# Optimization experiments

Measured on AMD Instinct MI355X. Metric: run time of the kernel, lower is better.

## Reference

```python
import jax, jax.numpy as jnp
import numpy as np

GRID_SIZE = 8
SPLINE_ORDER = 3
LAYERS = [256, 512, 512, 256]  # [input_dim] + hidden_dims
BATCH = 8192
BN_EPS = 1e-5


def make_grid(in_features):
    # efficient-kan/torchkan grid: uniform on [-1, 1] extended by spline_order on each side
    h = 2.0 / GRID_SIZE
    g = jnp.arange(-SPLINE_ORDER, GRID_SIZE + SPLINE_ORDER + 1, dtype=jnp.float32) * h - 1.0
    return jnp.broadcast_to(g, (in_features, g.shape[0]))  # (In, G + 2k + 1)


def b_splines(x, grid):
    # x: (B, In), grid: (In, G + 2k + 1) -> bases: (B, In, G + k)
    xg = x[:, :, None]
    bases = ((xg >= grid[:, :-1]) & (xg < grid[:, 1:])).astype(x.dtype)
    for k in range(1, SPLINE_ORDER + 1):
        left = (xg - grid[:, : -(k + 1)]) / (grid[:, k:-1] - grid[:, : -(k + 1)])
        right = (grid[:, k + 1 :] - xg) / (grid[:, k + 1 :] - grid[:, 1:-k])
        bases = left * bases[:, :, :-1] + right * bases[:, :, 1:]
    return bases


def kan_linear(x, grid, base_w, spline_w):
    # base path: GELU (exact, matching torch.nn.GELU) then linear
    base_out = jax.nn.gelu(x, approximate=False) @ base_w.T
    spline_out = jnp.einsum('bik,oik->bo', b_splines(x, grid), spline_w)
    return base_out + spline_out


def setup_inputs() -> dict:
    key = jax.random.key(0)
    ks = jax.random.split(key, 16)
    inp = {'x': jax.random.normal(ks[0], (BATCH, LAYERS[0]), dtype=jnp.float32)}
    n_bases = GRID_SIZE + SPLINE_ORDER
    for i, (fin, fout) in enumerate(zip(LAYERS[:-1], LAYERS[1:])):
        scale = 1.0 / np.sqrt(fin)
        inp[f'grid{i}'] = make_grid(fin)
        inp[f'base_w{i}'] = jax.random.normal(ks[1 + 3 * i], (fout, fin), dtype=jnp.float32) * scale
        inp[f'spline_w{i}'] = jax.random.normal(ks[2 + 3 * i], (fout, fin, n_bases), dtype=jnp.float32) * (0.1 * scale)
    d_out = LAYERS[-1]
    inp['bn_gamma'] = jnp.ones((d_out,), dtype=jnp.float32)
    inp['bn_beta'] = jnp.zeros((d_out,), dtype=jnp.float32)
    inp['bn_mean'] = jax.random.normal(ks[10], (d_out,), dtype=jnp.float32) * 0.1
    inp['bn_var'] = jax.random.uniform(ks[11], (d_out,), dtype=jnp.float32, minval=0.5, maxval=1.5)
    return inp


def reference(x, grid0, base_w0, spline_w0, grid1, base_w1, spline_w1, grid2, base_w2, spline_w2, bn_gamma, bn_beta, bn_mean, bn_var):
    h = kan_linear(x, grid0, base_w0, spline_w0)
    h = kan_linear(h, grid1, base_w1, spline_w1)
    h = kan_linear(h, grid2, base_w2, spline_w2)
    # BatchNorm1d in eval mode (running stats); Dropout is identity at inference
    return bn_gamma * (h - bn_mean) * jax.lax.rsqrt(bn_var + BN_EPS) + bn_beta
```

## Files before the change

kernel.cpp:

```cpp
#include <hip/hip_runtime.h>
#include <hip/hip_bf16.h>
#include <cstdint>


typedef unsigned short ushort_t;
typedef __bf16 bf16x8 __attribute__((ext_vector_type(8)));
typedef float f32x4 __attribute__((ext_vector_type(4)));
typedef _Float16 f16x4 __attribute__((ext_vector_type(4)));

__device__ __forceinline__ ushort_t f2bf(float f) {
    __bf16 h = (__bf16)f;
    return __builtin_bit_cast(ushort_t, h);
}

__device__ __forceinline__ void gload_lds16(const void* g, void* lds) {
    __builtin_amdgcn_global_load_lds(
        (const __attribute__((address_space(1))) unsigned int*)(uintptr_t)g,
        (__attribute__((address_space(3))) unsigned int*)(unsigned int)(uintptr_t)lds,
        16, 0, 0);
}

__device__ __forceinline__ void expand12(float x, ushort_t* o) {
    float x3 = x * x * x;
    float y  = 0.7978845608028654f * (x + 0.044715f * x3);
    float e  = __expf(2.0f * y);
    float th = 1.0f - 2.0f / (e + 1.0f);
    o[0] = f2bf(0.5f * x * (1.0f + th));
    float xs = (x + 1.75f) * 4.0f;
#pragma unroll
    for (int j = 0; j < 11; ++j) {
        float t  = xs - (float)j;
        float a  = fabsf(t - 2.0f);
        float p1 = (3.0f * a - 6.0f) * a * a + 4.0f;
        float c  = 2.0f - a;
        float p2 = c * c * c;
        float v  = (a <= 1.0f) ? p1 : fmaxf(p2, 0.0f);
        o[1 + j] = f2bf(v * (1.0f / 6.0f));
    }
}

__global__ __launch_bounds__(256) void expand_kernel(
    const float* __restrict__ X0, ushort_t* __restrict__ A, int total2)
{
    int idx = blockIdx.x * 256 + threadIdx.x;
    if (idx >= total2) return;
    float2 h = *(const float2*)(X0 + 2 * (size_t)idx);
    union { ushort_t us[24]; uint4 v[3]; } pk;
    expand12(h.x, pk.us);
    expand12(h.y, pk.us + 12);
    uint4* dst = (uint4*)(A + (size_t)idx * 24);
    dst[0] = pk.v[0]; dst[1] = pk.v[1]; dst[2] = pk.v[2];
}

__global__ __launch_bounds__(256) void expand_sum_kernel(
    const _Float16* __restrict__ P, size_t pstride,
    ushort_t* __restrict__ A, int total4)
{
    int idx = blockIdx.x * 256 + threadIdx.x;
    if (idx >= total4) return;
    float h0 = 0.f, h1 = 0.f, h2 = 0.f, h3 = 0.f;
#pragma unroll
    for (int s = 0; s < 4; ++s) {
        f16x4 v = *(const f16x4*)(P + s * pstride + 4 * (size_t)idx);
        h0 += (float)v.x; h1 += (float)v.y; h2 += (float)v.z; h3 += (float)v.w;
    }
    union { ushort_t us[48]; uint4 v[6]; } pk;
    expand12(h0, pk.us);
    expand12(h1, pk.us + 12);
    expand12(h2, pk.us + 24);
    expand12(h3, pk.us + 36);
    uint4* dst = (uint4*)(A + (size_t)idx * 48);
#pragma unroll
    for (int i = 0; i < 6; ++i) dst[i] = pk.v[i];
}

__global__ __launch_bounds__(256) void pack_w_kernel(
    const float* __restrict__ bw, const float* __restrict__ sw,
    ushort_t* __restrict__ W, int total)
{
    int idx = blockIdx.x * 256 + threadIdx.x;
    if (idx >= total) return;
    union { ushort_t us[12]; uint2 v[3]; } pk;
    pk.us[0] = f2bf(bw[idx]);
    const float* s = sw + (size_t)idx * 11;
#pragma unroll
    for (int k = 0; k < 11; ++k) pk.us[1 + k] = f2bf(s[k]);
    uint2* dst = (uint2*)(W + (size_t)idx * 12);
    dst[0] = pk.v[0]; dst[1] = pk.v[1]; dst[2] = pk.v[2];
}

#define SLOTE 16384

__global__ __launch_bounds__(512, 2) void gemm_kernel(
    const ushort_t* __restrict__ A,
    const ushort_t* __restrict__ W,
    _Float16* __restrict__ C,
    int M, int N, int K, int scps)
{
    extern __shared__ __align__(16) ushort_t lds[];

    const int t   = threadIdx.x;
    const int l   = t & 63;
    const int w   = t >> 6;
    const int wm  = w >> 2;
    const int wn  = w & 3;
    const int l15 = l & 15;
    const int q   = l >> 4;
    const int blockM = blockIdx.x * 256;
    const int blockN = blockIdx.y * 256;
    const int kb0 = blockIdx.z * scps;
    const int nt  = scps;
    _Float16* Cz = C + (size_t)blockIdx.z * M * N;

    const ushort_t* Ab = A + (size_t)blockM * K;
    const ushort_t* Wb = W + (size_t)blockN * K;

    auto stage = [&](int kb, int slot) {
        ushort_t* da = lds + slot * SLOTE;
        ushort_t* db = da + 8192;
#pragma unroll
        for (int it = 0; it < 2; ++it) {
            int s = it * 512 + t;
            int row = s >> 2, g = (s & 3) ^ ((row >> 1) & 3);
            gload_lds16(Ab + ((size_t)row * K + (kb << 5) + g * 8), da + s * 8);
        }
#pragma unroll
        for (int it = 0; it < 2; ++it) {
            int s = it * 512 + t;
            int row = s >> 2, g = (s & 3) ^ ((row >> 1) & 3);
            gload_lds16(Wb + ((size_t)row * K + (kb << 5) + g * 8), db + s * 8);
        }
    };

    auto ldfrags = [&](int slot, bf16x8* afr, bf16x8* bfr) {
        const ushort_t* Ac = lds + slot * SLOTE;
        const ushort_t* Bc = Ac + 8192;
#pragma unroll
        for (int ni = 0; ni < 4; ++ni) {
            int n = wn * 64 + ni * 16 + l15;
            bfr[ni] = *(const bf16x8*)&Bc[(size_t)((n << 2) + (q ^ ((n >> 1) & 3))) * 8];
        }
#pragma unroll
        for (int mi = 0; mi < 8; ++mi) {
            int m = wm * 128 + mi * 16 + l15;
            afr[mi] = *(const bf16x8*)&Ac[(size_t)((m << 2) + (q ^ ((m >> 1) & 3))) * 8];
        }
    };

    f32x4 acc[8][4];
#pragma unroll
    for (int i = 0; i < 8; ++i)
#pragma unroll
        for (int j = 0; j < 4; ++j) acc[i][j] = (f32x4){0.f, 0.f, 0.f, 0.f};

    stage(kb0 + 0, 0); stage(kb0 + 1, 1); stage(kb0 + 2, 2);
    asm volatile("s_waitcnt vmcnt(4)" ::: "memory");
    __builtin_amdgcn_s_barrier();

    bf16x8 aA[8], bA[4], aB[8], bB[4];
    ldfrags(0, aA, bA);
    asm volatile("s_waitcnt lgkmcnt(0)" ::: "memory");

    auto body = [&](int tt, bf16x8* ac, bf16x8* bc, bf16x8* an, bf16x8* bn) {
        if (tt + 3 < nt) stage(kb0 + tt + 3, (tt + 3) & 3);
        if (tt + 1 < nt) ldfrags((tt + 1) & 3, an, bn);
        __builtin_amdgcn_sched_barrier(0);
        __builtin_amdgcn_s_setprio(1);
#pragma unroll
        for (int mi = 0; mi < 8; ++mi)
#pragma unroll
            for (int ni = 0; ni < 4; ++ni)
                acc[mi][ni] = __builtin_amdgcn_mfma_f32_16x16x32_bf16(
                    ac[mi], bc[ni], acc[mi][ni], 0, 0, 0);
        __builtin_amdgcn_s_setprio(0);
        asm volatile("s_waitcnt lgkmcnt(0)" ::: "memory");
        if (tt + 3 < nt)      asm volatile("s_waitcnt vmcnt(4)" ::: "memory");
        else if (tt + 2 < nt) asm volatile("s_waitcnt vmcnt(0)" ::: "memory");
        __builtin_amdgcn_s_barrier();
    };

    for (int tt = 0; tt < nt; tt += 2) {
        body(tt,     aA, bA, aB, bB);
        body(tt + 1, aB, bB, aA, bA);
    }

#pragma unroll
    for (int ni = 0; ni < 4; ++ni) {
        int n = blockN + wn * 64 + ni * 16 + l15;
#pragma unroll
        for (int mi = 0; mi < 8; ++mi) {
            int mb = blockM + wm * 128 + mi * 16 + q * 4;
#pragma unroll
            for (int r = 0; r < 4; ++r)
                Cz[(size_t)(mb + r) * N + n] = (_Float16)acc[mi][ni][r];
        }
    }
}

__global__ __launch_bounds__(256) void bn_reduce_kernel(
    const _Float16* __restrict__ Q, size_t qstride,
    const float* __restrict__ gamma, const float* __restrict__ beta,
    const float* __restrict__ mean,  const float* __restrict__ var,
    float4* __restrict__ out, int n4)
{
    int i = blockIdx.x * 256 + threadIdx.x;
    if (i >= n4) return;
    float sx = 0.f, sy = 0.f, sz = 0.f, sw = 0.f;
#pragma unroll
    for (int s = 0; s < 8; ++s) {
        f16x4 v = *(const f16x4*)(Q + s * qstride + 4 * (size_t)i);
        sx += (float)v.x; sy += (float)v.y; sz += (float)v.z; sw += (float)v.w;
    }
    int nb = (i * 4) & 255;
    float4 g  = *(const float4*)(gamma + nb);
    float4 be = *(const float4*)(beta + nb);
    float4 mn = *(const float4*)(mean + nb);
    float4 vr = *(const float4*)(var + nb);
    float4 o;
    o.x = g.x * rsqrtf(vr.x + 1e-5f) * (sx - mn.x) + be.x;
    o.y = g.y * rsqrtf(vr.y + 1e-5f) * (sy - mn.y) + be.y;
    o.z = g.z * rsqrtf(vr.z + 1e-5f) * (sz - mn.z) + be.z;
    o.w = g.w * rsqrtf(vr.w + 1e-5f) * (sw - mn.w) + be.w;
    out[i] = o;
}

extern "C" void kernel_launch(void* const* d_in, const int* in_sizes, int n_in,
                              void* d_out, int out_size, void* d_ws, size_t ws_size,
                              hipStream_t stream) {
    const float* x     = (const float*)d_in[0];
    const float* bw0   = (const float*)d_in[2];
    const float* sw0   = (const float*)d_in[3];
    const float* bw1   = (const float*)d_in[5];
    const float* sw1   = (const float*)d_in[6];
    const float* bw2   = (const float*)d_in[8];
    const float* sw2   = (const float*)d_in[9];
    const float* gamma = (const float*)d_in[10];
    const float* beta  = (const float*)d_in[11];
    const float* mean  = (const float*)d_in[12];
    const float* var   = (const float*)d_in[13];

    char* ws = (char*)d_ws;
    ushort_t*  Abuf = (ushort_t*)(ws);
    ushort_t*  W0   = (ushort_t*)(ws + 100663296);
    ushort_t*  W1   = (ushort_t*)(ws + 103809024);
    ushort_t*  W2   = (ushort_t*)(ws + 110100480);
    _Float16*  P    = (_Float16*)(ws + 113246208);
    float*     out  = (float*)d_out;

    const size_t PS01 = (size_t)8192 * 512;
    const size_t PS2  = (size_t)8192 * 256;
    const size_t GEMM_LDS = 4 * SLOTE * sizeof(ushort_t);

    pack_w_kernel<<<(512 * 256 + 255) / 256, 256, 0, stream>>>(bw0, sw0, W0, 512 * 256);
    pack_w_kernel<<<(512 * 512 + 255) / 256, 256, 0, stream>>>(bw1, sw1, W1, 512 * 512);
    pack_w_kernel<<<(256 * 512 + 255) / 256, 256, 0, stream>>>(bw2, sw2, W2, 256 * 512);

    expand_kernel<<<4096, 256, 0, stream>>>(x, Abuf, 8192 * 256 / 2);
    {
        dim3 g(32, 2, 4);
        gemm_kernel<<<g, 512, GEMM_LDS, stream>>>(Abuf, W0, P, 8192, 512, 3072, 24);
    }
    expand_sum_kernel<<<4096, 256, 0, stream>>>(P, PS01, Abuf, 8192 * 512 / 4);
    {
        dim3 g(32, 2, 4);
        gemm_kernel<<<g, 512, GEMM_LDS, stream>>>(Abuf, W1, P, 8192, 512, 6144, 48);
    }
    expand_sum_kernel<<<4096, 256, 0, stream>>>(P, PS01, Abuf, 8192 * 512 / 4);
    {
        dim3 g(32, 1, 8);
        gemm_kernel<<<g, 512, GEMM_LDS, stream>>>(Abuf, W2, P, 8192, 256, 6144, 24);
    }
    bn_reduce_kernel<<<2048, 256, 0, stream>>>(
        P, PS2, gamma, beta, mean, var, (float4*)out, 8192 * 256 / 4);
}
```

Before: 326.3 us.

## Store expanded activation in K-block tiled panels for contiguous GEMM staging

The expand kernels now write the bf16 basis-expanded activation as 256-row by 32-column tiles, contiguous per K-block, instead of row-major. Each GEMM stage then reads one contiguous 16KB chunk for A rather than 256 rows strided by K, which should improve DRAM and TLB locality for the global-to-LDS loads. The expand kernel is reworked so each thread emits exactly one 32-element chunk. That chunk straddles feature boundaries and needs 3 or 4 feature expansions, so some expansion work is recomputed and the expand kernel's input reads become less coalesced.

```diff
diff --git a/kernel.cpp b/kernel.cpp
--- a/kernel.cpp
+++ b/kernel.cpp
@@ -39,39 +39,58 @@
     }
 }
 
-__global__ __launch_bounds__(256) void expand_kernel(
-    const float* __restrict__ X0, ushort_t* __restrict__ A, int total2)
-{
-    int idx = blockIdx.x * 256 + threadIdx.x;
-    if (idx >= total2) return;
-    float2 h = *(const float2*)(X0 + 2 * (size_t)idx);
-    union { ushort_t us[24]; uint4 v[3]; } pk;
-    expand12(h.x, pk.us);
-    expand12(h.y, pk.us + 12);
-    uint4* dst = (uint4*)(A + (size_t)idx * 24);
-    dst[0] = pk.v[0]; dst[1] = pk.v[1]; dst[2] = pk.v[2];
-}
-
-__global__ __launch_bounds__(256) void expand_sum_kernel(
-    const _Float16* __restrict__ P, size_t pstride,
-    ushort_t* __restrict__ A, int total4)
-{
-    int idx = blockIdx.x * 256 + threadIdx.x;
-    if (idx >= total4) return;
+__device__ __forceinline__ void pack32(const ushort_t* s, uint4* o) {
+#pragma unroll
+    for (int c = 0; c < 4; ++c) {
+        o[c].x = (unsigned)s[c * 8 + 0] | ((unsigned)s[c * 8 + 1] << 16);
+        o[c].y = (unsigned)s[c * 8 + 2] | ((unsigned)s[c * 8 + 3] << 16);
+        o[c].z = (unsigned)s[c * 8 + 4] | ((unsigned)s[c * 8 + 5] << 16);
+        o[c].w = (unsigned)s[c * 8 + 6] | ((unsigned)s[c * 8 + 7] << 16);
+    }
+}
+
+template <int KB, bool FROMX>
+__global__ __launch_bounds__(256) void expand_tiled_kernel(
+    const float* __restrict__ X, const _Float16* __restrict__ P,
+    size_t pstride, ushort_t* __restrict__ A)
+{
+    constexpr int F = KB * 8 / 3;
+    const int idx = blockIdx.x * 256 + threadIdx.x;
+    const int row = idx & 255;
+    const int pkb = idx >> 8;
+    const int kb  = pkb % KB;
+    const int p   = pkb / KB;
+    const int b   = p * 256 + row;
+    const int i0  = (kb * 8) / 3;
+    const int cse = kb - 3 * (kb / 3);
+
     float h0 = 0.f, h1 = 0.f, h2 = 0.f, h3 = 0.f;
-#pragma unroll
-    for (int s = 0; s < 4; ++s) {
-        f16x4 v = *(const f16x4*)(P + s * pstride + 4 * (size_t)idx);
-        h0 += (float)v.x; h1 += (float)v.y; h2 += (float)v.z; h3 += (float)v.w;
-    }
-    union { ushort_t us[48]; uint4 v[6]; } pk;
-    expand12(h0, pk.us);
-    expand12(h1, pk.us + 12);
-    expand12(h2, pk.us + 24);
-    expand12(h3, pk.us + 36);
-    uint4* dst = (uint4*)(A + (size_t)idx * 48);
-#pragma unroll
-    for (int i = 0; i < 6; ++i) dst[i] = pk.v[i];
+    if (FROMX) {
+        const float* xr = X + (size_t)b * F + i0;
+        h0 = xr[0]; h1 = xr[1]; h2 = xr[2];
+        if (cse == 1) h3 = xr[3];
+    } else {
+#pragma unroll
+        for (int z = 0; z < 4; ++z) {
+            const _Float16* pr = P + z * pstride + (size_t)b * F + i0;
+            h0 += (float)pr[0]; h1 += (float)pr[1]; h2 += (float)pr[2];
+            if (cse == 1) h3 += (float)pr[3];
+        }
+    }
+
+    ushort_t us[48];
+    expand12(h0, us);
+    expand12(h1, us + 12);
+    expand12(h2, us + 24);
+    if (cse == 1) expand12(h3, us + 36);
+
+    uint4 o[4];
+    if (cse == 0)      pack32(us + 0, o);
+    else if (cse == 1) pack32(us + 8, o);
+    else               pack32(us + 4, o);
+
+    uint4* dst = (uint4*)(A + (size_t)idx * 32);
+    dst[0] = o[0]; dst[1] = o[1]; dst[2] = o[2]; dst[3] = o[3];
 }
 
 __global__ __launch_bounds__(256) void pack_w_kernel(
@@ -95,7 +114,7 @@
     const ushort_t* __restrict__ A,
     const ushort_t* __restrict__ W,
     _Float16* __restrict__ C,
-    int M, int N, int K, int scps)
+    int M, int N, int KBT, int scps)
 {
     extern __shared__ __align__(16) ushort_t lds[];
 
@@ -106,29 +125,30 @@
     const int wn  = w & 3;
     const int l15 = l & 15;
     const int q   = l >> 4;
-    const int blockM = blockIdx.x * 256;
+    const int K   = KBT << 5;
     const int blockN = blockIdx.y * 256;
     const int kb0 = blockIdx.z * scps;
     const int nt  = scps;
     _Float16* Cz = C + (size_t)blockIdx.z * M * N;
 
-    const ushort_t* Ab = A + (size_t)blockM * K;
-    const ushort_t* Wb = W + (size_t)blockN * K;
+    const ushort_t* Apan = A + (size_t)blockIdx.x * KBT * 8192;
+    const ushort_t* Wb   = W + (size_t)blockN * K;
 
     auto stage = [&](int kb, int slot) {
         ushort_t* da = lds + slot * SLOTE;
         ushort_t* db = da + 8192;
+        const ushort_t* sa = Apan + (size_t)kb * 8192;
 #pragma unroll
         for (int it = 0; it < 2; ++it) {
             int s = it * 512 + t;
             int row = s >> 2, g = (s & 3) ^ ((row >> 1) & 3);
-            gload_lds16(Ab + ((size_t)row * K + (kb << 5) + g * 8), da + s * 8);
+            gload_lds16(sa + (row << 5) + (g << 3), da + s * 8);
         }
 #pragma unroll
         for (int it = 0; it < 2; ++it) {
             int s = it * 512 + t;
             int row = s >> 2, g = (s & 3) ^ ((row >> 1) & 3);
-            gload_lds16(Wb + ((size_t)row * K + (kb << 5) + g * 8), db + s * 8);
+            gload_lds16(Wb + ((size_t)row * K + (kb << 5) + (g << 3)), db + s * 8);
         }
     };
 
@@ -184,6 +204,7 @@
         body(tt + 1, aB, bB, aA, bA);
     }
 
+    const int blockM = blockIdx.x * 256;
 #pragma unroll
     for (int ni = 0; ni < 4; ++ni) {
         int n = blockN + wn * 64 + ni * 16 + l15;
@@ -255,20 +276,20 @@
     pack_w_kernel<<<(512 * 512 + 255) / 256, 256, 0, stream>>>(bw1, sw1, W1, 512 * 512);
     pack_w_kernel<<<(256 * 512 + 255) / 256, 256, 0, stream>>>(bw2, sw2, W2, 256 * 512);
 
-    expand_kernel<<<4096, 256, 0, stream>>>(x, Abuf, 8192 * 256 / 2);
+    expand_tiled_kernel<96, true><<<32 * 96, 256, 0, stream>>>(x, nullptr, 0, Abuf);
     {
         dim3 g(32, 2, 4);
-        gemm_kernel<<<g, 512, GEMM_LDS, stream>>>(Abuf, W0, P, 8192, 512, 3072, 24);
-    }
-    expand_sum_kernel<<<4096, 256, 0, stream>>>(P, PS01, Abuf, 8192 * 512 / 4);
+        gemm_kernel<<<g, 512, GEMM_LDS, stream>>>(Abuf, W0, P, 8192, 512, 96, 24);
+    }
+    expand_tiled_kernel<192, false><<<32 * 192, 256, 0, stream>>>(nullptr, P, PS01, Abuf);
     {
         dim3 g(32, 2, 4);
-        gemm_kernel<<<g, 512, GEMM_LDS, stream>>>(Abuf, W1, P, 8192, 512, 6144, 48);
-    }
-    expand_sum_kernel<<<4096, 256, 0, stream>>>(P, PS01, Abuf, 8192 * 512 / 4);
+        gemm_kernel<<<g, 512, GEMM_LDS, stream>>>(Abuf, W1, P, 8192, 512, 192, 48);
+    }
+    expand_tiled_kernel<192, false><<<32 * 192, 256, 0, stream>>>(nullptr, P, PS01, Abuf);
     {
         dim3 g(32, 1, 8);
-        gemm_kernel<<<g, 512, GEMM_LDS, stream>>>(Abuf, W2, P, 8192, 256, 6144, 24);
+        gemm_kernel<<<g, 512, GEMM_LDS, stream>>>(Abuf, W2, P, 8192, 256, 192, 24);
     }
     bn_reduce_kernel<<<2048, 256, 0, stream>>>(
         P, PS2, gamma, beta, mean, var, (float4*)out, 8192 * 256 / 4);
```

Result: slower. 410.9 us (+25.9%).
